# Performance work log

Hardware: AMD Instinct MI355X
Metric: run time of the kernel (lower is better)

Reference implementation:

```python
import math
import jax, jax.numpy as jnp
import numpy as np

B, S, H, D = 2, 2048, 16, 64

def setup_inputs() -> dict:
    key = jax.random.key(0)
    kq, kk, kv = jax.random.split(key, 3)
    query = jax.random.normal(kq, (B, S, H, D), dtype=jnp.float32)
    k_ = jax.random.normal(kk, (B, S, H, D), dtype=jnp.float32)
    v_ = jax.random.normal(kv, (B, S, H, D), dtype=jnp.float32)
    return {"query": query, "key": k_, "value": v_}

def reference(query, key, value):
    # USPAttention.__call__ with req=None -> simple_attention, causal=False
    scale = 1.0 / math.sqrt(query.shape[-1])
    q = jnp.transpose(query, (0, 2, 1, 3))  # [B,H,S,D]
    k = jnp.transpose(key, (0, 2, 1, 3))
    v = jnp.transpose(value, (0, 2, 1, 3))
    attn = jnp.einsum('bhsd,bhtd->bhst', q, k) * scale  # [B,H,S,S]
    attn = jax.nn.softmax(attn, axis=-1)
    out = jnp.einsum('bhst,bhtd->bhsd', attn, v)
    return jnp.transpose(out, (0, 2, 1, 3))  # [B,S,H,D]
```

## Files before the change

### kernel.cpp

```cpp
#include <hip/hip_runtime.h>
#include <hip/hip_bf16.h>
#include <math.h>

typedef float f32x4 __attribute__((ext_vector_type(4)));
typedef short s16x8 __attribute__((ext_vector_type(8)));

#define NS 2048
#define NH 16
#define ND 64
#define QTILE 128
#define KVB 64
#define NT (NS / KVB)
#define QSCALE 0.18033688f
#define DEFER_THR 11.5f

__device__ __forceinline__ unsigned cvtpk(float lo, float hi) {
    unsigned r;
    asm("v_cvt_pk_bf16_f32 %0, %1, %2" : "=v"(r) : "v"(lo), "v"(hi));
    return r;
}

__global__ __launch_bounds__(512, 4)
void usp_attn(const float* __restrict__ Qg, const float* __restrict__ Kg,
              const float* __restrict__ Vg, float* __restrict__ Og) {
    __shared__ unsigned short Klds[2][64 * 64];
    __shared__ unsigned short Vt[2][64 * 64];
    __shared__ unsigned short Plds[8][16 * 64];

    const int tid  = threadIdx.x;
    const int w    = tid >> 6;
    const int lane = tid & 63;
    const int g    = lane >> 4;
    const int x    = lane & 15;

    int bid = blockIdx.x;
    int wg  = (bid & 7) * 64 + (bid >> 3);
    int qt  = wg & 15;
    int bh  = wg >> 4;
    int b   = bh >> 4;
    int h   = bh & 15;
    int q0  = qt * QTILE;

    const int srow = NH * ND;
    const size_t base = ((size_t)b * NS * NH + h) * ND;

    const int qrow = q0 + w * 16 + x;
    const float* qp = Qg + base + (size_t)qrow * srow;
    s16x8 qf[2];
#pragma unroll
    for (int ks = 0; ks < 2; ++ks) {
        int d0 = ks * 32 + g * 8;
        f32x4 a = *(const f32x4*)(qp + d0);
        f32x4 c = *(const f32x4*)(qp + d0 + 4);
        union { s16x8 v; unsigned u[4]; } r;
        r.u[0] = cvtpk(a[0] * QSCALE, a[1] * QSCALE);
        r.u[1] = cvtpk(a[2] * QSCALE, a[3] * QSCALE);
        r.u[2] = cvtpk(c[0] * QSCALE, c[1] * QSCALE);
        r.u[3] = cvtpk(c[2] * QSCALE, c[3] * QSCALE);
        qf[ks] = r.v;
    }

    f32x4 oacc[4];
#pragma unroll
    for (int dt = 0; dt < 4; ++dt) oacc[dt] = f32x4{0.f, 0.f, 0.f, 0.f};
    float mrun = -INFINITY, lrun = 0.f;

    const int sub = tid >> 4;
    const int c4  = (tid & 15) * 4;
    const float* kb = Kg + base + (size_t)sub * srow + c4;
    const float* vb = Vg + base + (size_t)sub * srow + c4;

    f32x4 kreg[2], vreg[2];
#define LOADT(t) do { \
        size_t off = (size_t)(t) * KVB * srow; \
        kreg[0] = *(const f32x4*)(kb + off); \
        kreg[1] = *(const f32x4*)(kb + off + (size_t)32 * srow); \
        vreg[0] = *(const f32x4*)(vb + off); \
        vreg[1] = *(const f32x4*)(vb + off + (size_t)32 * srow); \
    } while (0)

#define STORET(bf) do { \
        _Pragma("unroll") \
        for (int p = 0; p < 2; ++p) { \
            int kv = sub + 32 * p; \
            int de = c4 ^ ((kv & 7) << 3); \
            *(uint2*)(&Klds[bf][kv * 64 + de]) = \
                uint2{cvtpk(kreg[p][0], kreg[p][1]), cvtpk(kreg[p][2], kreg[p][3])}; \
            unsigned va = cvtpk(vreg[p][0], vreg[p][1]); \
            unsigned vb2 = cvtpk(vreg[p][2], vreg[p][3]); \
            int s01 = kv ^ (((c4 >> 1) & 7) << 3); \
            int s23 = kv ^ ((((c4 >> 1) + 1) & 7) << 3); \
            Vt[bf][(c4 + 0) * 64 + s01] = (unsigned short)va; \
            Vt[bf][(c4 + 1) * 64 + s01] = (unsigned short)(va >> 16); \
            Vt[bf][(c4 + 2) * 64 + s23] = (unsigned short)vb2; \
            Vt[bf][(c4 + 3) * 64 + s23] = (unsigned short)(vb2 >> 16); \
        } \
    } while (0)

    LOADT(0);
    STORET(0);
    LOADT(1);
    __syncthreads();

    unsigned short* Pw = &Plds[w][0];
    const int rsw = (x & 7) << 3;
    const int vsw = (x >> 1) << 3;

    for (int t = 0; t < NT; ++t) {
        const unsigned short* Kc = &Klds[t & 1][0];
        const unsigned short* Vc = &Vt[t & 1][0];

        if (t + 1 < NT) STORET((t + 1) & 1);
        if (t + 2 < NT) LOADT(t + 2);

        f32x4 sc[4];
#pragma unroll
        for (int nt = 0; nt < 4; ++nt) sc[nt] = f32x4{0.f, 0.f, 0.f, 0.f};
        __builtin_amdgcn_s_setprio(1);
#pragma unroll
        for (int nt = 0; nt < 4; ++nt) {
            int krow = (16 * nt + x) * 64;
#pragma unroll
            for (int ks = 0; ks < 2; ++ks) {
                s16x8 kf = *(const s16x8*)(&Kc[krow + ((32 * ks + 8 * g) ^ rsw)]);
                sc[nt] = __builtin_amdgcn_mfma_f32_16x16x32_bf16(kf, qf[ks], sc[nt], 0, 0, 0);
            }
        }
        __builtin_amdgcn_s_setprio(0);

        float mx = sc[0][0];
#pragma unroll
        for (int nt = 0; nt < 4; ++nt)
#pragma unroll
            for (int r = 0; r < 4; ++r) mx = fmaxf(mx, sc[nt][r]);
        mx = fmaxf(mx, __shfl_xor(mx, 16));
        mx = fmaxf(mx, __shfl_xor(mx, 32));
        if (!__all(mx - mrun <= DEFER_THR)) {
            float mnew = fmaxf(mrun, mx);
            float alpha = exp2f(mrun - mnew);
            mrun = mnew;
            lrun *= alpha;
#pragma unroll
            for (int dt = 0; dt < 4; ++dt)
#pragma unroll
                for (int r = 0; r < 4; ++r) oacc[dt][r] *= alpha;
        }
        float rs = 0.f;
#pragma unroll
        for (int nt = 0; nt < 4; ++nt) {
            float p0 = exp2f(sc[nt][0] - mrun);
            float p1 = exp2f(sc[nt][1] - mrun);
            float p2 = exp2f(sc[nt][2] - mrun);
            float p3 = exp2f(sc[nt][3] - mrun);
            rs += (p0 + p1) + (p2 + p3);
            *(uint2*)(&Pw[x * 64 + ((16 * nt + 4 * g) ^ rsw)]) =
                uint2{cvtpk(p0, p1), cvtpk(p2, p3)};
        }
        rs += __shfl_xor(rs, 16);
        rs += __shfl_xor(rs, 32);
        lrun += rs;

        __builtin_amdgcn_s_setprio(1);
#pragma unroll
        for (int ks = 0; ks < 2; ++ks) {
            int k0 = 32 * ks + 8 * g;
            s16x8 pf = *(const s16x8*)(&Pw[x * 64 + (k0 ^ rsw)]);
#pragma unroll
            for (int dt = 0; dt < 4; ++dt) {
                s16x8 vf = *(const s16x8*)(&Vc[(16 * dt + x) * 64 + (k0 ^ vsw)]);
                oacc[dt] = __builtin_amdgcn_mfma_f32_16x16x32_bf16(vf, pf, oacc[dt], 0, 0, 0);
            }
        }
        __builtin_amdgcn_s_setprio(0);

        __syncthreads();
    }

    float inv = 1.0f / lrun;
    float* op = Og + base + (size_t)qrow * srow;
#pragma unroll
    for (int dt = 0; dt < 4; ++dt) {
        f32x4 r = oacc[dt];
        r[0] *= inv; r[1] *= inv; r[2] *= inv; r[3] *= inv;
        *(f32x4*)(op + 16 * dt + 4 * g) = r;
    }
}

extern "C" void kernel_launch(void* const* d_in, const int* in_sizes, int n_in,
                              void* d_out, int out_size, void* d_ws, size_t ws_size,
                              hipStream_t stream) {
    const float* Q = (const float*)d_in[0];
    const float* K = (const float*)d_in[1];
    const float* V = (const float*)d_in[2];
    float* O = (float*)d_out;
    usp_attn<<<dim3(512), dim3(512), 0, stream>>>(Q, K, V, O);
}
```

Baseline: 153.9 us.

## Process two 16-row query tiles per wave to reuse K/V fragments

Doubles the query tile per workgroup from 128 to 256 rows, so each wave now owns two 16-row m-tiles with separate softmax state and accumulators. Each K and V fragment read from LDS now feeds two MFMAs, and each block's global K/V load and bf16 conversion is shared by twice as many queries. The grid is halved to 256 blocks and launch bounds drop to 2 blocks per SM. The trade is higher register pressure and fewer resident waves per CU to hide latency, with the whole CU stalling at each barrier.

```diff
diff --git a/kernel.cpp b/kernel.cpp
--- a/kernel.cpp
+++ b/kernel.cpp
@@ -8,7 +8,7 @@
 #define NS 2048
 #define NH 16
 #define ND 64
-#define QTILE 128
+#define QTILE 256
 #define KVB 64
 #define NT (NS / KVB)
 #define QSCALE 0.18033688f
@@ -20,12 +20,12 @@
     return r;
 }
 
-__global__ __launch_bounds__(512, 4)
+__global__ __launch_bounds__(512, 2)
 void usp_attn(const float* __restrict__ Qg, const float* __restrict__ Kg,
               const float* __restrict__ Vg, float* __restrict__ Og) {
     __shared__ unsigned short Klds[2][64 * 64];
     __shared__ unsigned short Vt[2][64 * 64];
-    __shared__ unsigned short Plds[8][16 * 64];
+    __shared__ unsigned short Plds[8][2 * 16 * 64];
 
     const int tid  = threadIdx.x;
     const int w    = tid >> 6;
@@ -34,9 +34,9 @@
     const int x    = lane & 15;
 
     int bid = blockIdx.x;
-    int wg  = (bid & 7) * 64 + (bid >> 3);
-    int qt  = wg & 15;
-    int bh  = wg >> 4;
+    int wg  = (bid & 7) * 32 + (bid >> 3);
+    int qt  = wg & 7;
+    int bh  = wg >> 3;
     int b   = bh >> 4;
     int h   = bh & 15;
     int q0  = qt * QTILE;
@@ -44,26 +44,30 @@
     const int srow = NH * ND;
     const size_t base = ((size_t)b * NS * NH + h) * ND;
 
-    const int qrow = q0 + w * 16 + x;
-    const float* qp = Qg + base + (size_t)qrow * srow;
-    s16x8 qf[2];
-#pragma unroll
-    for (int ks = 0; ks < 2; ++ks) {
-        int d0 = ks * 32 + g * 8;
-        f32x4 a = *(const f32x4*)(qp + d0);
-        f32x4 c = *(const f32x4*)(qp + d0 + 4);
-        union { s16x8 v; unsigned u[4]; } r;
-        r.u[0] = cvtpk(a[0] * QSCALE, a[1] * QSCALE);
-        r.u[1] = cvtpk(a[2] * QSCALE, a[3] * QSCALE);
-        r.u[2] = cvtpk(c[0] * QSCALE, c[1] * QSCALE);
-        r.u[3] = cvtpk(c[2] * QSCALE, c[3] * QSCALE);
-        qf[ks] = r.v;
+    s16x8 qf[2][2];
+#pragma unroll
+    for (int mt = 0; mt < 2; ++mt) {
+        const float* qp = Qg + base + (size_t)(q0 + w * 32 + mt * 16 + x) * srow;
+#pragma unroll
+        for (int ks = 0; ks < 2; ++ks) {
+            int d0 = ks * 32 + g * 8;
+            f32x4 a = *(const f32x4*)(qp + d0);
+            f32x4 c = *(const f32x4*)(qp + d0 + 4);
+            union { s16x8 v; unsigned u[4]; } r;
+            r.u[0] = cvtpk(a[0] * QSCALE, a[1] * QSCALE);
+            r.u[1] = cvtpk(a[2] * QSCALE, a[3] * QSCALE);
+            r.u[2] = cvtpk(c[0] * QSCALE, c[1] * QSCALE);
+            r.u[3] = cvtpk(c[2] * QSCALE, c[3] * QSCALE);
+            qf[mt][ks] = r.v;
+        }
     }
 
-    f32x4 oacc[4];
-#pragma unroll
-    for (int dt = 0; dt < 4; ++dt) oacc[dt] = f32x4{0.f, 0.f, 0.f, 0.f};
-    float mrun = -INFINITY, lrun = 0.f;
+    f32x4 oacc[2][4];
+    float mrun[2] = {-INFINITY, -INFINITY}, lrun[2] = {0.f, 0.f};
+#pragma unroll
+    for (int mt = 0; mt < 2; ++mt)
+#pragma unroll
+        for (int dt = 0; dt < 4; ++dt) oacc[mt][dt] = f32x4{0.f, 0.f, 0.f, 0.f};
 
     const int sub = tid >> 4;
     const int c4  = (tid & 15) * 4;
@@ -113,62 +117,70 @@
         if (t + 1 < NT) STORET((t + 1) & 1);
         if (t + 2 < NT) LOADT(t + 2);
 
-        f32x4 sc[4];
-#pragma unroll
-        for (int nt = 0; nt < 4; ++nt) sc[nt] = f32x4{0.f, 0.f, 0.f, 0.f};
+        f32x4 sc[2][4];
+#pragma unroll
+        for (int mt = 0; mt < 2; ++mt)
+#pragma unroll
+            for (int nt = 0; nt < 4; ++nt) sc[mt][nt] = f32x4{0.f, 0.f, 0.f, 0.f};
         __builtin_amdgcn_s_setprio(1);
 #pragma unroll
         for (int nt = 0; nt < 4; ++nt) {
             int krow = (16 * nt + x) * 64;
-#pragma unroll
-            for (int ks = 0; ks < 2; ++ks) {
-                s16x8 kf = *(const s16x8*)(&Kc[krow + ((32 * ks + 8 * g) ^ rsw)]);
-                sc[nt] = __builtin_amdgcn_mfma_f32_16x16x32_bf16(kf, qf[ks], sc[nt], 0, 0, 0);
+            s16x8 kf0 = *(const s16x8*)(&Kc[krow + ((8 * g) ^ rsw)]);
+            s16x8 kf1 = *(const s16x8*)(&Kc[krow + ((32 + 8 * g) ^ rsw)]);
+            sc[0][nt] = __builtin_amdgcn_mfma_f32_16x16x32_bf16(kf0, qf[0][0], sc[0][nt], 0, 0, 0);
+            sc[0][nt] = __builtin_amdgcn_mfma_f32_16x16x32_bf16(kf1, qf[0][1], sc[0][nt], 0, 0, 0);
+            sc[1][nt] = __builtin_amdgcn_mfma_f32_16x16x32_bf16(kf0, qf[1][0], sc[1][nt], 0, 0, 0);
+            sc[1][nt] = __builtin_amdgcn_mfma_f32_16x16x32_bf16(kf1, qf[1][1], sc[1][nt], 0, 0, 0);
+        }
+        __builtin_amdgcn_s_setprio(0);
+
+#pragma unroll
+        for (int mt = 0; mt < 2; ++mt) {
+            float mx = sc[mt][0][0];
+#pragma unroll
+            for (int nt = 0; nt < 4; ++nt)
+#pragma unroll
+                for (int r = 0; r < 4; ++r) mx = fmaxf(mx, sc[mt][nt][r]);
+            mx = fmaxf(mx, __shfl_xor(mx, 16));
+            mx = fmaxf(mx, __shfl_xor(mx, 32));
+            if (!__all(mx - mrun[mt] <= DEFER_THR)) {
+                float mnew = fmaxf(mrun[mt], mx);
+                float alpha = exp2f(mrun[mt] - mnew);
+                mrun[mt] = mnew;
+                lrun[mt] *= alpha;
+#pragma unroll
+                for (int dt = 0; dt < 4; ++dt)
+#pragma unroll
+                    for (int r = 0; r < 4; ++r) oacc[mt][dt][r] *= alpha;
             }
-        }
-        __builtin_amdgcn_s_setprio(0);
-
-        float mx = sc[0][0];
-#pragma unroll
-        for (int nt = 0; nt < 4; ++nt)
-#pragma unroll
-            for (int r = 0; r < 4; ++r) mx = fmaxf(mx, sc[nt][r]);
-        mx = fmaxf(mx, __shfl_xor(mx, 16));
-        mx = fmaxf(mx, __shfl_xor(mx, 32));
-        if (!__all(mx - mrun <= DEFER_THR)) {
-            float mnew = fmaxf(mrun, mx);
-            float alpha = exp2f(mrun - mnew);
-            mrun = mnew;
-            lrun *= alpha;
-#pragma unroll
-            for (int dt = 0; dt < 4; ++dt)
-#pragma unroll
-                for (int r = 0; r < 4; ++r) oacc[dt][r] *= alpha;
-        }
-        float rs = 0.f;
-#pragma unroll
-        for (int nt = 0; nt < 4; ++nt) {
-            float p0 = exp2f(sc[nt][0] - mrun);
-            float p1 = exp2f(sc[nt][1] - mrun);
-            float p2 = exp2f(sc[nt][2] - mrun);
-            float p3 = exp2f(sc[nt][3] - mrun);
-            rs += (p0 + p1) + (p2 + p3);
-            *(uint2*)(&Pw[x * 64 + ((16 * nt + 4 * g) ^ rsw)]) =
-                uint2{cvtpk(p0, p1), cvtpk(p2, p3)};
-        }
-        rs += __shfl_xor(rs, 16);
-        rs += __shfl_xor(rs, 32);
-        lrun += rs;
+            float rs = 0.f;
+#pragma unroll
+            for (int nt = 0; nt < 4; ++nt) {
+                float p0 = exp2f(sc[mt][nt][0] - mrun[mt]);
+                float p1 = exp2f(sc[mt][nt][1] - mrun[mt]);
+                float p2 = exp2f(sc[mt][nt][2] - mrun[mt]);
+                float p3 = exp2f(sc[mt][nt][3] - mrun[mt]);
+                rs += (p0 + p1) + (p2 + p3);
+                *(uint2*)(&Pw[mt * 1024 + x * 64 + ((16 * nt + 4 * g) ^ rsw)]) =
+                    uint2{cvtpk(p0, p1), cvtpk(p2, p3)};
+            }
+            rs += __shfl_xor(rs, 16);
+            rs += __shfl_xor(rs, 32);
+            lrun[mt] += rs;
+        }
 
         __builtin_amdgcn_s_setprio(1);
 #pragma unroll
         for (int ks = 0; ks < 2; ++ks) {
             int k0 = 32 * ks + 8 * g;
-            s16x8 pf = *(const s16x8*)(&Pw[x * 64 + (k0 ^ rsw)]);
+            s16x8 pf0 = *(const s16x8*)(&Pw[x * 64 + (k0 ^ rsw)]);
+            s16x8 pf1 = *(const s16x8*)(&Pw[1024 + x * 64 + (k0 ^ rsw)]);
 #pragma unroll
             for (int dt = 0; dt < 4; ++dt) {
                 s16x8 vf = *(const s16x8*)(&Vc[(16 * dt + x) * 64 + (k0 ^ vsw)]);
-                oacc[dt] = __builtin_amdgcn_mfma_f32_16x16x32_bf16(vf, pf, oacc[dt], 0, 0, 0);
+                oacc[0][dt] = __builtin_amdgcn_mfma_f32_16x16x32_bf16(vf, pf0, oacc[0][dt], 0, 0, 0);
+                oacc[1][dt] = __builtin_amdgcn_mfma_f32_16x16x32_bf16(vf, pf1, oacc[1][dt], 0, 0, 0);
             }
         }
         __builtin_amdgcn_s_setprio(0);
@@ -176,13 +188,16 @@
         __syncthreads();
     }
 
-    float inv = 1.0f / lrun;
-    float* op = Og + base + (size_t)qrow * srow;
-#pragma unroll
-    for (int dt = 0; dt < 4; ++dt) {
-        f32x4 r = oacc[dt];
-        r[0] *= inv; r[1] *= inv; r[2] *= inv; r[3] *= inv;
-        *(f32x4*)(op + 16 * dt + 4 * g) = r;
+#pragma unroll
+    for (int mt = 0; mt < 2; ++mt) {
+        float inv = 1.0f / lrun[mt];
+        float* op = Og + base + (size_t)(q0 + w * 32 + mt * 16 + x) * srow;
+#pragma unroll
+        for (int dt = 0; dt < 4; ++dt) {
+            f32x4 r = oacc[mt][dt];
+            r[0] *= inv; r[1] *= inv; r[2] *= inv; r[3] *= inv;
+            *(f32x4*)(op + 16 * dt + 4 * g) = r;
+        }
     }
 }
 
@@ -193,5 +208,5 @@
     const float* K = (const float*)d_in[1];
     const float* V = (const float*)d_in[2];
     float* O = (float*)d_out;
-    usp_attn<<<dim3(512), dim3(512), 0, stream>>>(Q, K, V, O);
+    usp_attn<<<dim3(256), dim3(512), 0, stream>>>(Q, K, V, O);
 }
```

New measurement: 156.1 us. About the same (+1.4%).
